# Performance work log

Measured on AMD Instinct MI355X. Metric: run time of the kernel, lower is better.

Reference implementation:

```python
import jax, jax.numpy as jnp
import numpy as np

B, C, D, N, NCLS = 2048, 96, 384, 200000, 10
LN_EPS = 1e-5


def setup_inputs() -> dict:
    key = jax.random.key(0)
    ks = jax.random.split(key, 16)
    s = 0.05  # keep squared-distance logits in a sane range
    inp = {
        'k': jax.random.normal(ks[0], (B, D), jnp.float32) * s,
        'context_idx': jax.random.randint(ks[1], (B, C), 0, N),
        'candidate_embeddings': jax.random.normal(ks[2], (N, D), jnp.float32) * s,
        'candidate_y': jax.random.randint(ks[3], (N,), 0, NCLS),
        # learned params
        'label_emb': jax.random.normal(ks[4], (NCLS, D), jnp.float32) * 0.02,
        'ln_g': jnp.ones((D,), jnp.float32),
        'ln_b': jnp.zeros((D,), jnp.float32),
        'kp_w1': jax.random.normal(ks[5], (D, D), jnp.float32) * (1.0 / np.sqrt(D)),
        'kp_b1': jnp.zeros((D,), jnp.float32),
        'kp_w2': jax.random.normal(ks[6], (D, D), jnp.float32) * (1.0 / np.sqrt(D)),
        'kp_b2': jnp.zeros((D,), jnp.float32),
        'pw1': jax.random.normal(ks[7], (D, D), jnp.float32) * (1.0 / np.sqrt(D)),
        'pb1': jnp.zeros((D,), jnp.float32),
        'pw2': jax.random.normal(ks[8], (D, NCLS), jnp.float32) * (1.0 / np.sqrt(D)),
        'pb2': jnp.zeros((NCLS,), jnp.float32),
    }
    return inp


def reference(k, context_idx, candidate_embeddings, candidate_y,
              label_emb, ln_g, ln_b, kp_w1, kp_b1, kp_w2, kp_b2,
              pw1, pb1, pw2, pb2):
    # gather context (irregular access): [B, C, D], [B, C]
    context_k = candidate_embeddings[context_idx]
    context_y = candidate_y[context_idx]

    # negative squared distance via kernel trick: -|k|^2 + 2 k.ck - |ck|^2
    sim = (-jnp.sum(k * k, axis=-1, keepdims=True)
           + 2.0 * jnp.einsum('bd,bcd->bc', k, context_k)
           - jnp.sum(context_k * context_k, axis=-1))  # [B, C]
    probs = jax.nn.softmax(sim, axis=-1)  # dropout is identity in eval mode

    context_y_emb = label_emb[context_y]  # [B, C, D]

    # key_proj: LayerNorm -> Linear -> SiLU -> Linear, residual (d_main==n_out)
    def key_proj(x):
        mu = jnp.mean(x, axis=-1, keepdims=True)
        var = jnp.mean(jnp.square(x - mu), axis=-1, keepdims=True)
        h = (x - mu) * jax.lax.rsqrt(var + LN_EPS) * ln_g + ln_b
        h = jax.nn.silu(h @ kp_w1 + kp_b1)
        h = h @ kp_w2 + kp_b2
        return x + h

    # Abl == -1 branch: values = label_emb + key_proj(k - context_k)
    values = context_y_emb + key_proj(k[:, None, :] - context_k)  # [B, C, D]

    # probs[:, None] @ values -> weighted sum over context
    context_x = jnp.einsum('bc,bcd->bd', probs, values)
    x = k + context_x

    # predictor MLP (no residual: d_main != n_classes)
    h = jax.nn.silu(x @ pw1 + pb1)
    y = h @ pw2 + pb2
    return y
```

## Files before the change

### kernel.cpp

```cpp
#include <hip/hip_runtime.h>
#include <hip/hip_bf16.h>

#define BB   2048
#define CC   96
#define DD   384
#define NCLSS 10
#define AS_STRIDE 392

typedef __attribute__((ext_vector_type(8))) __bf16 bf16x8;
typedef __attribute__((ext_vector_type(4))) float  floatx4;
typedef unsigned int  uint32;
typedef unsigned short ushort16;
typedef __attribute__((ext_vector_type(4))) uint32 uintx4;

__device__ __forceinline__ float bflo(uint32 u){ return __uint_as_float(u << 16); }
__device__ __forceinline__ float bfhi(uint32 u){ return __uint_as_float(u & 0xffff0000u); }
__device__ __forceinline__ float bf1(ushort16 s){ return __uint_as_float(((uint32)s) << 16); }
__device__ __forceinline__ ushort16 f2bf(float f){
  uint32 u = __float_as_uint(f);
  return (ushort16)((u + 0x7fffu + ((u >> 16) & 1u)) >> 16);
}
__device__ __forceinline__ int probe_f32(const void* lng_raw){
  return (((const uint32*)lng_raw)[0] == 0x3F800000u) ? 1 : 0;
}
__device__ __forceinline__ float ld1(const void* p, size_t i, int isf32){
  return isf32 ? ((const float*)p)[i] : bf1(((const ushort16*)p)[i]);
}

__global__ __launch_bounds__(256) void k_canon(
    const void* w1, const void* w2, const void* pw1,
    const void* lng, const void* lnb, const void* b1,
    ushort16* __restrict__ wW1T, ushort16* __restrict__ wW2T,
    ushort16* __restrict__ wPW1T,
    float* __restrict__ sconst, float* __restrict__ tconst)
{
  int isf32 = probe_f32(lng);
  if (blockIdx.x >= 432) {
    __shared__ float sred[8][32], tred[8][32];
    int bid = blockIdx.x - 432;
    int nl = threadIdx.x & 31, jl = threadIdx.x >> 5;
    int n = bid * 32 + nl;
    float s = 0.f, tt = 0.f;
    for (int j = jl; j < DD; j += 8) {
      float w = ld1(w1, (size_t)j * DD + n, isf32);
      s  += ld1(lng, j, isf32) * w;
      tt += ld1(lnb, j, isf32) * w;
    }
    sred[jl][nl] = s; tred[jl][nl] = tt;
    __syncthreads();
    if (jl == 0) {
      #pragma unroll
      for (int r = 1; r < 8; r++) { s += sred[r][nl]; tt += tred[r][nl]; }
      sconst[n] = s;
      tconst[n] = tt + ld1(b1, n, isf32);
    }
    return;
  }
  int m  = blockIdx.x / 144;
  int t  = blockIdx.x % 144;
  int tr = t / 12, tc = t % 12;
  const void* src = (m == 0) ? w1 : (m == 1) ? w2 : pw1;
  ushort16* dst   = (m == 0) ? wW1T : (m == 1) ? wW2T : wPW1T;
  __shared__ float tile[32][33];
  int tx = threadIdx.x & 31, ty = threadIdx.x >> 5;
  #pragma unroll
  for (int p = 0; p < 4; p++)
    tile[p*8 + ty][tx] = ld1(src, (size_t)(tr*32 + p*8 + ty) * DD + tc*32 + tx, isf32);
  __syncthreads();
  float gmul = (m == 0) ? ld1(lng, tr*32 + tx, isf32) : 1.f;
  #pragma unroll
  for (int p = 0; p < 4; p++)
    dst[(size_t)(tc*32 + p*8 + ty) * DD + tr*32 + tx] = f2bf(tile[tx][p*8 + ty] * gmul);
}

__global__ __launch_bounds__(512, 4) void k_fused(
    const void* kptr, const int* __restrict__ cidx,
    const void* cand, const int* __restrict__ cy,
    const void* lng,
    const ushort16* __restrict__ w1t,
    const float* __restrict__ sconst, const float* __restrict__ tconst,
    float* __restrict__ wxpre, float* __restrict__ wpl, float* __restrict__ wsum)
{
  int isf32 = probe_f32(lng);
  int b = blockIdx.x;
  int tid = threadIdx.x, wave = tid >> 6, lane = tid & 63;
  int t = lane & 15, kq = lane >> 4;
  __shared__ __align__(16) char AsB[96 * 768];
  __shared__ __align__(16) float ksh[DD];
  __shared__ float sims[CC], probs[CC], rsigv[CC], rmuv[CC];
  __shared__ float plbuf[NCLSS], xacc[DD];

  if (tid < NCLSS) plbuf[tid] = 0.f;
  if (tid < DD) {
    xacc[tid] = 0.f;
    ksh[tid]  = ld1(kptr, (size_t)b * DD + tid, isf32);
  }

  int tr_ = (t < 12) ? t : t - 12;
  int c  = wave * 12 + tr_;
  int idx = cidx[b * CC + c];
  int swz = (c & 7) << 4;
  __syncthreads();

  float s1 = 0.f, s2 = 0.f;
  if (!isf32) {
    const uintx4* cp = (const uintx4*)((const ushort16*)cand + (size_t)idx * DD);
    uintx4 ckr[12];
    #pragma unroll
    for (int kt = 0; kt < 12; kt++) ckr[kt] = cp[kt*4 + kq];
    #pragma unroll
    for (int kt = 0; kt < 12; kt++) {
      int j0 = kt*32 + kq*8;
      floatx4 ka = *(const floatx4*)&ksh[j0];
      floatx4 kb = *(const floatx4*)&ksh[j0+4];
      float kk[8] = {ka[0],ka[1],ka[2],ka[3],kb[0],kb[1],kb[2],kb[3]};
      float ck[8] = {bflo(ckr[kt][0]),bfhi(ckr[kt][0]),bflo(ckr[kt][1]),bfhi(ckr[kt][1]),
                     bflo(ckr[kt][2]),bfhi(ckr[kt][2]),bflo(ckr[kt][3]),bfhi(ckr[kt][3])};
      uint32 w[4];
      #pragma unroll
      for (int p = 0; p < 4; p++) {
        float d0 = kk[2*p]   - ck[2*p];
        float d1 = kk[2*p+1] - ck[2*p+1];
        s1 += d0 + d1; s2 += d0*d0 + d1*d1;
        w[p] = (uint32)f2bf(d0) | ((uint32)f2bf(d1) << 16);
      }
      if (t < 12) {
        uintx4 vv = { w[0], w[1], w[2], w[3] };
        *(uintx4*)(AsB + ((c * 768 + kt * 64 + kq * 16) ^ swz)) = vv;
      }
    }
  } else {
    const float* cf = (const float*)cand + (size_t)idx * DD;
    #pragma unroll
    for (int h = 0; h < 2; h++) {
      floatx4 cr[12];
      #pragma unroll
      for (int q = 0; q < 6; q++) {
        int j0 = (h*6+q)*32 + kq*8;
        cr[2*q]   = *(const floatx4*)(cf + j0);
        cr[2*q+1] = *(const floatx4*)(cf + j0 + 4);
      }
      #pragma unroll
      for (int q = 0; q < 6; q++) {
        int kt = h*6 + q;
        int j0 = kt*32 + kq*8;
        floatx4 ka = *(const floatx4*)&ksh[j0];
        floatx4 kb = *(const floatx4*)&ksh[j0+4];
        float kk[8] = {ka[0],ka[1],ka[2],ka[3],kb[0],kb[1],kb[2],kb[3]};
        float ck[8] = {cr[2*q][0],cr[2*q][1],cr[2*q][2],cr[2*q][3],
                       cr[2*q+1][0],cr[2*q+1][1],cr[2*q+1][2],cr[2*q+1][3]};
        uint32 w[4];
        #pragma unroll
        for (int p = 0; p < 4; p++) {
          float d0 = kk[2*p]   - ck[2*p];
          float d1 = kk[2*p+1] - ck[2*p+1];
          s1 += d0 + d1; s2 += d0*d0 + d1*d1;
          w[p] = (uint32)f2bf(d0) | ((uint32)f2bf(d1) << 16);
        }
        if (t < 12) {
          uintx4 vv = { w[0], w[1], w[2], w[3] };
          *(uintx4*)(AsB + ((c * 768 + kt * 64 + kq * 16) ^ swz)) = vv;
        }
      }
    }
  }
  s1 += __shfl_xor(s1, 16); s2 += __shfl_xor(s2, 16);
  s1 += __shfl_xor(s1, 32); s2 += __shfl_xor(s2, 32);
  float mu = s1 * (1.f/DD), var = s2 * (1.f/DD) - mu*mu;
  float rsig = rsqrtf(var + 1e-5f);
  if (kq == 0 && t < 12) { sims[c] = -s2; rsigv[c] = rsig; rmuv[c] = rsig * mu; }
  __syncthreads();

  if (wave == 0) {
    float v0 = sims[lane];
    float v1 = (lane < 32) ? sims[lane + 64] : -1e30f;
    float mx = fmaxf(v0, v1);
    #pragma unroll
    for (int m = 32; m; m >>= 1) mx = fmaxf(mx, __shfl_xor(mx, m));
    float e0 = __expf(v0 - mx);
    float e1 = (lane < 32) ? __expf(v1 - mx) : 0.f;
    float s = e0 + e1;
    #pragma unroll
    for (int m = 32; m; m >>= 1) s += __shfl_xor(s, m);
    float inv = 1.f / s;
    probs[lane] = e0 * inv;
    if (lane < 32) probs[lane + 64] = e1 * inv;
  }
  __syncthreads();

  if (tid < CC) atomicAdd(&plbuf[cy[cidx[b * CC + tid]]], probs[tid]);
  {
    float T0=0,T1=0,T2=0,T3=0,T4=0,T5=0;
    #pragma unroll
    for (int i = 0; i < 12; i++) {
      int cc = wave * 12 + i;
      float p = probs[cc];
      const char* rp = AsB + cc * 768;
      int sz = (cc & 7) << 4;
      uint32 a0 = *(const uint32*)(rp + ((lane*12 + 0) ^ sz));
      uint32 a1 = *(const uint32*)(rp + ((lane*12 + 4) ^ sz));
      uint32 a2 = *(const uint32*)(rp + ((lane*12 + 8) ^ sz));
      T0 += p*bflo(a0); T1 += p*bfhi(a0); T2 += p*bflo(a1);
      T3 += p*bfhi(a1); T4 += p*bflo(a2); T5 += p*bfhi(a2);
    }
    int j0 = lane * 6;
    atomicAdd(&xacc[j0+0], T0); atomicAdd(&xacc[j0+1], T1);
    atomicAdd(&xacc[j0+2], T2); atomicAdd(&xacc[j0+3], T3);
    atomicAdd(&xacc[j0+4], T4); atomicAdd(&xacc[j0+5], T5);
  }
  __syncthreads();

  if (tid < DD)
    wxpre[(size_t)b * DD + tid] = ksh[tid] + xacc[tid];
  if (tid < NCLSS) wpl[b * NCLSS + tid] = plbuf[tid];

  int col = lane & 15, quad = lane >> 4;
  int n0 = wave * 48;
  floatx4 acc[6][3];
  #pragma unroll
  for (int i = 0; i < 6; i++)
    #pragma unroll
    for (int j = 0; j < 3; j++) acc[i][j] = (floatx4)0.f;

  const ushort16* wbase = w1t + (size_t)(n0 + col) * DD + quad * 8;
  bf16x8 bcur[3];
  #pragma unroll
  for (int tn = 0; tn < 3; tn++)
    bcur[tn] = *(const bf16x8*)(wbase + (size_t)tn * 16 * DD);
  #pragma unroll 1
  for (int kt = 0; kt < 12; kt++) {
    bf16x8 bnxt[3] = { (bf16x8)0, (bf16x8)0, (bf16x8)0 };
    if (kt < 11) {
      #pragma unroll
      for (int tn = 0; tn < 3; tn++)
        bnxt[tn] = *(const bf16x8*)(wbase + (size_t)tn * 16 * DD + (kt+1) * 32);
    }
    #pragma unroll
    for (int tm = 0; tm < 6; tm++) {
      int r = tm*16 + col;
      bf16x8 afrag = *(const bf16x8*)(AsB + ((r * 768 + kt*64 + quad*16) ^ ((r & 7) << 4)));
      #pragma unroll
      for (int tn = 0; tn < 3; tn++)
        acc[tm][tn] = __builtin_amdgcn_mfma_f32_16x16x32_bf16(afrag, bcur[tn], acc[tm][tn], 0, 0, 0);
    }
    #pragma unroll
    for (int tn = 0; tn < 3; tn++) bcur[tn] = bnxt[tn];
  }

  #pragma unroll
  for (int tn = 0; tn < 3; tn++) {
    int n = n0 + tn*16 + col;
    float sn = sconst[n], tnc = tconst[n];
    float val = 0.f;
    #pragma unroll
    for (int tm = 0; tm < 6; tm++) {
      #pragma unroll
      for (int r = 0; r < 4; r++) {
        int row = tm*16 + quad*4 + r;
        float h = rsigv[row] * acc[tm][tn][r] - rmuv[row] * sn + tnc;
        h = h / (1.f + __expf(-h));
        val += probs[row] * h;
      }
    }
    val += __shfl_xor(val, 16);
    val += __shfl_xor(val, 32);
    if (quad == 0) wsum[(size_t)b * DD + n] = val;
  }
}

__global__ __launch_bounds__(512) void k_final(
    const float* __restrict__ wxpre, const float* __restrict__ wsum,
    const float* __restrict__ wpl, const void* lemb,
    const ushort16* __restrict__ w2t, const void* b2,
    const ushort16* __restrict__ pw1t, const void* pb1,
    const void* pw2, const void* pb2,
    const void* lng_raw, void* out)
{
  int isf32 = probe_f32(lng_raw);
  int b0 = blockIdx.x * 8;
  int tid = threadIdx.x, wave = tid >> 6, lane = tid & 63;
  int cn = lane & 15, quad = lane >> 4;
  __shared__ __align__(16) ushort16 As[16 * AS_STRIDE];
  __shared__ float hbuf[8][AS_STRIDE];
  __shared__ float lembsh[NCLSS * DD];
  __shared__ float plsh[8][NCLSS];
  __shared__ float part[480];

  for (int e = tid; e < 16 * AS_STRIDE; e += 512) {
    int r = e / AS_STRIDE, j = e - r * AS_STRIDE;
    ushort16 v = (ushort16)0;
    if (r < 8 && j < DD) v = f2bf(wsum[(size_t)(b0 + r) * DD + j]);
    As[e] = v;
  }
  for (int e = tid; e < NCLSS * DD; e += 512) lembsh[e] = ld1(lemb, e, isf32);
  if (tid < 80) plsh[tid / NCLSS][tid % NCLSS] = wpl[(b0 + tid / NCLSS) * NCLSS + tid % NCLSS];
  __syncthreads();

  int n0 = wave * 48;
  floatx4 acc[3];
  #pragma unroll
  for (int j = 0; j < 3; j++) acc[j] = (floatx4)0.f;
  const ushort16* wb2 = w2t + (size_t)(n0 + cn) * DD + quad * 8;
  #pragma unroll 2
  for (int kt = 0; kt < 12; kt++) {
    bf16x8 afrag = *(const bf16x8*)(As + cn * AS_STRIDE + kt*32 + quad*8);
    #pragma unroll
    for (int tn = 0; tn < 3; tn++) {
      bf16x8 bfrag = *(const bf16x8*)(wb2 + (size_t)tn * 16 * DD + kt * 32);
      acc[tn] = __builtin_amdgcn_mfma_f32_16x16x32_bf16(afrag, bfrag, acc[tn], 0, 0, 0);
    }
  }
  float xv[3][4];
  #pragma unroll
  for (int tn = 0; tn < 3; tn++) {
    int n = n0 + tn*16 + cn;
    float bb = ld1(b2, n, isf32);
    #pragma unroll
    for (int r = 0; r < 4; r++) {
      int row = quad*4 + r;
      if (row < 8) {
        float v = acc[tn][r] + bb + wxpre[(size_t)(b0 + row) * DD + n];
        #pragma unroll
        for (int l = 0; l < NCLSS; l++) v += plsh[row][l] * lembsh[l * DD + n];
        xv[tn][r] = v;
      }
    }
  }
  __syncthreads();
  #pragma unroll
  for (int tn = 0; tn < 3; tn++) {
    int n = n0 + tn*16 + cn;
    #pragma unroll
    for (int r = 0; r < 4; r++) {
      int row = quad*4 + r;
      if (row < 8) As[row * AS_STRIDE + n] = f2bf(xv[tn][r]);
    }
  }
  __syncthreads();

  floatx4 acc2[3];
  #pragma unroll
  for (int j = 0; j < 3; j++) acc2[j] = (floatx4)0.f;
  const ushort16* wbp = pw1t + (size_t)(n0 + cn) * DD + quad * 8;
  #pragma unroll 2
  for (int kt = 0; kt < 12; kt++) {
    bf16x8 afrag = *(const bf16x8*)(As + cn * AS_STRIDE + kt*32 + quad*8);
    #pragma unroll
    for (int tn = 0; tn < 3; tn++) {
      bf16x8 bfrag = *(const bf16x8*)(wbp + (size_t)tn * 16 * DD + kt * 32);
      acc2[tn] = __builtin_amdgcn_mfma_f32_16x16x32_bf16(afrag, bfrag, acc2[tn], 0, 0, 0);
    }
  }
  #pragma unroll
  for (int tn = 0; tn < 3; tn++) {
    int n = n0 + tn*16 + cn;
    float bb = ld1(pb1, n, isf32);
    #pragma unroll
    for (int r = 0; r < 4; r++) {
      int row = quad*4 + r;
      if (row < 8) {
        float h = acc2[tn][r] + bb;
        hbuf[row][n] = h / (1.f + __expf(-h));
      }
    }
  }
  __syncthreads();

  if (tid < 480) {
    int r = tid / 60, rem = tid % 60, n = rem / 6, s = rem % 6;
    float pp = 0.f;
    int jb = s * 64;
    #pragma unroll 8
    for (int jj = 0; jj < 64; jj++) {
      int j = jb + jj;
      pp += hbuf[r][j] * ld1(pw2, (size_t)j * NCLSS + n, isf32);
    }
    part[tid] = pp;
  }
  __syncthreads();
  if (tid < 80) {
    int r = tid / NCLSS, n = tid % NCLSS;
    float y = ld1(pb2, n, isf32);
    #pragma unroll
    for (int s = 0; s < 6; s++) y += part[r*60 + n*6 + s];
    size_t o = (size_t)(b0 + r) * NCLSS + n;
    if (isf32) ((float*)out)[o] = y;
    else       ((ushort16*)out)[o] = f2bf(y);
  }
}

extern "C" void kernel_launch(void* const* d_in, const int* in_sizes, int n_in,
                              void* d_out, int out_size, void* d_ws, size_t ws_size,
                              hipStream_t stream) {
  const void* kptr = d_in[0];
  const int*  cidx = (const int*)d_in[1];
  const void* cand = d_in[2];
  const int*  cy   = (const int*)d_in[3];
  const void* lemb = d_in[4];
  const void* lng  = d_in[5];
  const void* lnb  = d_in[6];
  const void* w1   = d_in[7];
  const void* b1   = d_in[8];
  const void* w2   = d_in[9];
  const void* b2   = d_in[10];
  const void* pw1  = d_in[11];
  const void* pb1  = d_in[12];
  const void* pw2  = d_in[13];
  const void* pb2  = d_in[14];

  char* ws = (char*)d_ws;
  ushort16* wW1T   = (ushort16*)(ws);
  ushort16* wW2T   = (ushort16*)(ws + 294912);
  ushort16* wPW1T  = (ushort16*)(ws + 589824);
  float*    wxpre  = (float*)   (ws + 884736);
  float*    wpl    = (float*)   (ws + 4030464);
  float*    wsum   = (float*)   (ws + 4112384);
  float*    sconst = (float*)   (ws + 7258112);
  float*    tconst = (float*)   (ws + 7259648);

  k_canon<<<444, 256, 0, stream>>>(w1, w2, pw1, lng, lnb, b1,
                                   wW1T, wW2T, wPW1T, sconst, tconst);
  k_fused<<<BB, 512, 0, stream>>>(kptr, cidx, cand, cy, lng, wW1T,
                                  sconst, tconst, wxpre, wpl, wsum);
  k_final<<<256, 512, 0, stream>>>(wxpre, wsum, wpl, lemb, wW2T, b2,
                                   wPW1T, pb1, pw2, pb2, lng, d_out);
}
```

Before: 574.5 us.

## Split gather and k-load across waves, use packed bf16 convert and fast sigmoid

Restructures the gather phase so waves 0-5 each handle 16 context rows with no idle lanes, while waves 6-7 load the query vector into shared memory. The candidate gathers are issued before the barrier, so the global loads overlap the k load. The barrier is a raw lgkmcnt wait plus s_barrier, which avoids waiting on the outstanding vector memory loads. Float-to-bf16 rounding now uses the hardware v_cvt_pk_bf16_f32 instruction, and SiLU uses raw v_exp/v_rcp. The epilogue is reordered so per-row probs and LN stats are loaded once per row tile. Risks: inline asm can limit compiler scheduling, register pressure rises from holding the gathered rows across the barrier, and approximate exp/rcp changes precision slightly.

```diff
diff --git a/kernel.cpp b/kernel.cpp
--- a/kernel.cpp
+++ b/kernel.cpp
@@ -19,6 +19,18 @@
 __device__ __forceinline__ ushort16 f2bf(float f){
   uint32 u = __float_as_uint(f);
   return (ushort16)((u + 0x7fffu + ((u >> 16) & 1u)) >> 16);
+}
+__device__ __forceinline__ uint32 pk2bf(float lo, float hi){
+  uint32 r;
+  asm("v_cvt_pk_bf16_f32 %0, %1, %2" : "=v"(r) : "v"(lo), "v"(hi));
+  return r;
+}
+__device__ __forceinline__ float fast_sig(float h){
+  float e, rc;
+  asm("v_exp_f32 %0, %1" : "=v"(e) : "v"(h * -1.44269504089f));
+  float d = 1.f + e;
+  asm("v_rcp_f32 %0, %1" : "=v"(rc) : "v"(d));
+  return rc;
 }
 __device__ __forceinline__ int probe_f32(const void* lng_raw){
   return (((const uint32*)lng_raw)[0] == 0x3F800000u) ? 1 : 0;
@@ -91,84 +103,90 @@
   __shared__ float plbuf[NCLSS], xacc[DD];
 
   if (tid < NCLSS) plbuf[tid] = 0.f;
-  if (tid < DD) {
-    xacc[tid] = 0.f;
-    ksh[tid]  = ld1(kptr, (size_t)b * DD + tid, isf32);
-  }
-
-  int tr_ = (t < 12) ? t : t - 12;
-  int c  = wave * 12 + tr_;
-  int idx = cidx[b * CC + c];
+  if (tid < DD)    xacc[tid]  = 0.f;
+
+  int c  = wave * 16 + t;
   int swz = (c & 7) << 4;
-  __syncthreads();
+  int idx = 0;
+  uintx4  ckr[12];
+  floatx4 crf[12];
+
+  if (wave < 6) {
+    idx = cidx[b * CC + c];
+    if (!isf32) {
+      const uintx4* cp = (const uintx4*)((const ushort16*)cand + (size_t)idx * DD);
+      #pragma unroll
+      for (int kt = 0; kt < 12; kt++) ckr[kt] = cp[kt*4 + kq];
+    } else {
+      const float* cf = (const float*)cand + (size_t)idx * DD;
+      #pragma unroll
+      for (int q = 0; q < 6; q++) {
+        int j0 = q*32 + kq*8;
+        crf[2*q]   = *(const floatx4*)(cf + j0);
+        crf[2*q+1] = *(const floatx4*)(cf + j0 + 4);
+      }
+    }
+  } else {
+    int q = tid - 384;
+    #pragma unroll
+    for (int r = 0; r < 3; r++)
+      ksh[q + 128*r] = ld1(kptr, (size_t)b * DD + q + 128*r, isf32);
+  }
+  __builtin_amdgcn_sched_barrier(0);
+  asm volatile("s_waitcnt lgkmcnt(0)\n\ts_barrier" ::: "memory");
 
   float s1 = 0.f, s2 = 0.f;
-  if (!isf32) {
-    const uintx4* cp = (const uintx4*)((const ushort16*)cand + (size_t)idx * DD);
-    uintx4 ckr[12];
-    #pragma unroll
-    for (int kt = 0; kt < 12; kt++) ckr[kt] = cp[kt*4 + kq];
-    #pragma unroll
-    for (int kt = 0; kt < 12; kt++) {
-      int j0 = kt*32 + kq*8;
-      floatx4 ka = *(const floatx4*)&ksh[j0];
-      floatx4 kb = *(const floatx4*)&ksh[j0+4];
-      float kk[8] = {ka[0],ka[1],ka[2],ka[3],kb[0],kb[1],kb[2],kb[3]};
-      float ck[8] = {bflo(ckr[kt][0]),bfhi(ckr[kt][0]),bflo(ckr[kt][1]),bfhi(ckr[kt][1]),
-                     bflo(ckr[kt][2]),bfhi(ckr[kt][2]),bflo(ckr[kt][3]),bfhi(ckr[kt][3])};
-      uint32 w[4];
-      #pragma unroll
-      for (int p = 0; p < 4; p++) {
-        float d0 = kk[2*p]   - ck[2*p];
-        float d1 = kk[2*p+1] - ck[2*p+1];
-        s1 += d0 + d1; s2 += d0*d0 + d1*d1;
-        w[p] = (uint32)f2bf(d0) | ((uint32)f2bf(d1) << 16);
-      }
-      if (t < 12) {
-        uintx4 vv = { w[0], w[1], w[2], w[3] };
-        *(uintx4*)(AsB + ((c * 768 + kt * 64 + kq * 16) ^ swz)) = vv;
-      }
-    }
-  } else {
-    const float* cf = (const float*)cand + (size_t)idx * DD;
-    #pragma unroll
-    for (int h = 0; h < 2; h++) {
-      floatx4 cr[12];
-      #pragma unroll
-      for (int q = 0; q < 6; q++) {
-        int j0 = (h*6+q)*32 + kq*8;
-        cr[2*q]   = *(const floatx4*)(cf + j0);
-        cr[2*q+1] = *(const floatx4*)(cf + j0 + 4);
-      }
-      #pragma unroll
-      for (int q = 0; q < 6; q++) {
-        int kt = h*6 + q;
+  if (wave < 6) {
+    if (!isf32) {
+      #pragma unroll
+      for (int kt = 0; kt < 12; kt++) {
         int j0 = kt*32 + kq*8;
         floatx4 ka = *(const floatx4*)&ksh[j0];
         floatx4 kb = *(const floatx4*)&ksh[j0+4];
         float kk[8] = {ka[0],ka[1],ka[2],ka[3],kb[0],kb[1],kb[2],kb[3]};
-        float ck[8] = {cr[2*q][0],cr[2*q][1],cr[2*q][2],cr[2*q][3],
-                       cr[2*q+1][0],cr[2*q+1][1],cr[2*q+1][2],cr[2*q+1][3]};
-        uint32 w[4];
+        float ck[8] = {bflo(ckr[kt][0]),bfhi(ckr[kt][0]),bflo(ckr[kt][1]),bfhi(ckr[kt][1]),
+                       bflo(ckr[kt][2]),bfhi(ckr[kt][2]),bflo(ckr[kt][3]),bfhi(ckr[kt][3])};
+        float d[8];
         #pragma unroll
-        for (int p = 0; p < 4; p++) {
-          float d0 = kk[2*p]   - ck[2*p];
-          float d1 = kk[2*p+1] - ck[2*p+1];
-          s1 += d0 + d1; s2 += d0*d0 + d1*d1;
-          w[p] = (uint32)f2bf(d0) | ((uint32)f2bf(d1) << 16);
+        for (int j = 0; j < 8; j++) { d[j] = kk[j] - ck[j]; s1 += d[j]; s2 += d[j]*d[j]; }
+        uintx4 vv = { pk2bf(d[0],d[1]), pk2bf(d[2],d[3]), pk2bf(d[4],d[5]), pk2bf(d[6],d[7]) };
+        *(uintx4*)(AsB + ((c * 768 + kt * 64 + kq * 16) ^ swz)) = vv;
+      }
+    } else {
+      const float* cf = (const float*)cand + (size_t)idx * DD;
+      #pragma unroll
+      for (int h = 0; h < 2; h++) {
+        if (h == 1) {
+          #pragma unroll
+          for (int q = 0; q < 6; q++) {
+            int j0 = (6+q)*32 + kq*8;
+            crf[2*q]   = *(const floatx4*)(cf + j0);
+            crf[2*q+1] = *(const floatx4*)(cf + j0 + 4);
+          }
         }
-        if (t < 12) {
-          uintx4 vv = { w[0], w[1], w[2], w[3] };
+        #pragma unroll
+        for (int q = 0; q < 6; q++) {
+          int kt = h*6 + q;
+          int j0 = kt*32 + kq*8;
+          floatx4 ka = *(const floatx4*)&ksh[j0];
+          floatx4 kb = *(const floatx4*)&ksh[j0+4];
+          float kk[8] = {ka[0],ka[1],ka[2],ka[3],kb[0],kb[1],kb[2],kb[3]};
+          float ck[8] = {crf[2*q][0],crf[2*q][1],crf[2*q][2],crf[2*q][3],
+                         crf[2*q+1][0],crf[2*q+1][1],crf[2*q+1][2],crf[2*q+1][3]};
+          float d[8];
+          #pragma unroll
+          for (int j = 0; j < 8; j++) { d[j] = kk[j] - ck[j]; s1 += d[j]; s2 += d[j]*d[j]; }
+          uintx4 vv = { pk2bf(d[0],d[1]), pk2bf(d[2],d[3]), pk2bf(d[4],d[5]), pk2bf(d[6],d[7]) };
           *(uintx4*)(AsB + ((c * 768 + kt * 64 + kq * 16) ^ swz)) = vv;
         }
       }
     }
-  }
-  s1 += __shfl_xor(s1, 16); s2 += __shfl_xor(s2, 16);
-  s1 += __shfl_xor(s1, 32); s2 += __shfl_xor(s2, 32);
-  float mu = s1 * (1.f/DD), var = s2 * (1.f/DD) - mu*mu;
-  float rsig = rsqrtf(var + 1e-5f);
-  if (kq == 0 && t < 12) { sims[c] = -s2; rsigv[c] = rsig; rmuv[c] = rsig * mu; }
+    s1 += __shfl_xor(s1, 16); s2 += __shfl_xor(s2, 16);
+    s1 += __shfl_xor(s1, 32); s2 += __shfl_xor(s2, 32);
+    float mu = s1 * (1.f/DD), var = s2 * (1.f/DD) - mu*mu;
+    float rsig = rsqrtf(var + 1e-5f);
+    if (kq == 0) { sims[c] = -s2; rsigv[c] = rsig; rmuv[c] = rsig * mu; }
+  }
   __syncthreads();
 
   if (wave == 0) {
@@ -247,24 +265,35 @@
     for (int tn = 0; tn < 3; tn++) bcur[tn] = bnxt[tn];
   }
 
+  float snv[3], tnv[3], val[3];
   #pragma unroll
   for (int tn = 0; tn < 3; tn++) {
     int n = n0 + tn*16 + col;
-    float sn = sconst[n], tnc = tconst[n];
-    float val = 0.f;
-    #pragma unroll
-    for (int tm = 0; tm < 6; tm++) {
+    snv[tn] = sconst[n]; tnv[tn] = tconst[n]; val[tn] = 0.f;
+  }
+  #pragma unroll
+  for (int tm = 0; tm < 6; tm++) {
+    float pr[4], rs[4], rm[4];
+    #pragma unroll
+    for (int r = 0; r < 4; r++) {
+      int row = tm*16 + quad*4 + r;
+      pr[r] = probs[row]; rs[r] = rsigv[row]; rm[r] = rmuv[row];
+    }
+    #pragma unroll
+    for (int tn = 0; tn < 3; tn++) {
       #pragma unroll
       for (int r = 0; r < 4; r++) {
-        int row = tm*16 + quad*4 + r;
-        float h = rsigv[row] * acc[tm][tn][r] - rmuv[row] * sn + tnc;
-        h = h / (1.f + __expf(-h));
-        val += probs[row] * h;
-      }
-    }
-    val += __shfl_xor(val, 16);
-    val += __shfl_xor(val, 32);
-    if (quad == 0) wsum[(size_t)b * DD + n] = val;
+        float h = rs[r] * acc[tm][tn][r] - rm[r] * snv[tn] + tnv[tn];
+        val[tn] += pr[r] * (h * fast_sig(h));
+      }
+    }
+  }
+  #pragma unroll
+  for (int tn = 0; tn < 3; tn++) {
+    float v = val[tn];
+    v += __shfl_xor(v, 16);
+    v += __shfl_xor(v, 32);
+    if (quad == 0) wsum[(size_t)b * DD + n0 + tn*16 + col] = v;
   }
 }
 
```

New measurement: 583.2 us. No clear change (+1.5%).
